# Performance work log

Hardware: AMD Instinct MI355X
Metric: run time of the kernel (lower is better)

## Reference

```python
import jax, jax.numpy as jnp
import numpy as np

H = 16            # num heads
D = 64            # head dim
HID = 1024        # hidden size
ALPHA = 1.0       # < 2 -> power-law kernel
BANDWIDTH = 1.0
A = 0.5           # doubly-stochastic exponent
RADIUS = 1.0      # sphere radius
EPS = 1e-7


def setup_inputs() -> dict:
    key = jax.random.key(0)
    ks = jax.random.split(key, 5)
    x = jax.random.normal(ks[0], (2, 2048, HID), dtype=jnp.float32)
    s = 1.0 / np.sqrt(HID)
    qkv_w = jax.random.normal(ks[1], (3 * HID, HID), dtype=jnp.float32) * s
    qkv_b = jnp.zeros((3 * HID,), dtype=jnp.float32)
    out_w = jax.random.normal(ks[2], (HID, HID), dtype=jnp.float32) * s
    out_b = jnp.zeros((HID,), dtype=jnp.float32)
    return {"x": x, "qkv_w": qkv_w, "qkv_b": qkv_b, "out_w": out_w, "out_b": out_b}


def _l2norm(t):
    # torch F.normalize(p=2, dim=-1): divide by max(||t||, 1e-12)
    n = jnp.sqrt(jnp.sum(t * t, axis=-1, keepdims=True))
    return t / jnp.maximum(n, 1e-12)


def reference(x, qkv_w, qkv_b, out_w, out_b):
    B, S, _ = x.shape
    qkv = x @ qkv_w.T + qkv_b                       # [B,S,3*HID]
    q, k, v = jnp.split(qkv, 3, axis=-1)
    # [B,H,S,D]
    q = _l2norm(q.reshape(B, S, H, D).transpose(0, 2, 1, 3))
    k = _l2norm(k.reshape(B, S, H, D).transpose(0, 2, 1, 3))
    v = v.reshape(B, S, H, D).transpose(0, 2, 1, 3)
    # geodesic distance on the sphere
    cos = jnp.clip(jnp.einsum('bhsd,bhtd->bhst', q, k), -1.0 + EPS, 1.0 - EPS)
    g_dist = jnp.arccos(cos) * RADIUS               # [B,H,S,S]
    # alpha < 2: power-law kernel
    attn_score = (1.0 + g_dist / jnp.sqrt(BANDWIDTH)) ** (-(D + ALPHA))
    # doubly-stochastic-style rescale: diag(row^-a) @ K @ diag(col^-a)
    row = attn_score.sum(-1) ** (-A)                # [B,H,S]
    col = attn_score.sum(-2) ** (-A)                # [B,H,S]
    k_tilde = row[..., :, None] * attn_score * col[..., None, :]
    # F.normalize(p=1, dim=3): divide by max(sum |.|, 1e-12); entries >= 0
    probs = k_tilde / jnp.maximum(k_tilde.sum(-1, keepdims=True), 1e-12)
    out = jnp.einsum('bhst,bhtd->bhsd', probs, v)   # [B,H,S,D]
    out = out.transpose(0, 2, 1, 3).reshape(B, S, HID)
    return out @ out_w.T + out_b
```

## Files before the change

kernel.cpp:

```cpp
#include <hip/hip_runtime.h>
#include <math.h>

#define NH   16
#define HD   64
#define HIDN 1024
#define NB   2
#define SEQ  2048
#define ROWS (NB*SEQ)
#define BH   (NB*NH)

typedef __attribute__((ext_vector_type(8))) short bf16x8;
typedef __attribute__((ext_vector_type(8))) _Float16 f16x8;
typedef __attribute__((ext_vector_type(4))) float f32x4;
typedef _Float16 f16;

typedef const __attribute__((address_space(1))) void GV;
typedef __attribute__((address_space(3))) void LV;
__device__ __forceinline__ void glds16(const void* g, void* l) {
    __builtin_amdgcn_global_load_lds((GV*)g, (LV*)l, 16, 0, 0);
}

__device__ __forceinline__ unsigned short f2bf(float f) {
    unsigned u = __float_as_uint(f);
    u += 0x7FFF + ((u >> 16) & 1);
    return (unsigned short)(u >> 16);
}
__device__ __forceinline__ bf16x8 ldfrag(const unsigned short* p) {
    return *(const bf16x8*)p;
}
__device__ __forceinline__ f16x8 ldfragh(const f16* p) {
    return *(const f16x8*)p;
}
__device__ __forceinline__ f32x4 mfma16(bf16x8 a, bf16x8 b, f32x4 c) {
    return __builtin_amdgcn_mfma_f32_16x16x32_bf16(a, b, c, 0, 0, 0);
}
__device__ __forceinline__ f32x4 mfma16h(f16x8 a, f16x8 b, f32x4 c) {
    return __builtin_amdgcn_mfma_f32_16x16x32_f16(a, b, c, 0, 0, 0);
}

__device__ __forceinline__ float log2_1pacos(float c) {
    float u = fmaxf(1.0f - c, 0.0f);
    float s = __builtin_amdgcn_sqrtf(u);
    float p = fmaf(u, 2.68532e-3f, 7.89259e-3f);
    p = fmaf(u, p, 2.6516504e-2f);
    p = fmaf(u, p, 1.1785113e-1f);
    p = fmaf(u, p, 1.4142136f);
    return __builtin_amdgcn_logf(fmaf(s, p, 1.0f));
}

__global__ __launch_bounds__(256)
void conv_f16(const float* __restrict__ src, f16* __restrict__ dst) {
    int i = (blockIdx.x * 256 + threadIdx.x) * 8;
    float4 a = *(const float4*)(src + i);
    float4 b = *(const float4*)(src + i + 4);
    f16x8 o = { (f16)a.x, (f16)a.y, (f16)a.z, (f16)a.w,
                (f16)b.x, (f16)b.y, (f16)b.z, (f16)b.w };
    *(f16x8*)(dst + i) = o;
}

__global__ __launch_bounds__(256)
void gemm_nt_f16(const f16* __restrict__ A, const f16* __restrict__ B,
                 const float* __restrict__ bias, float* __restrict__ C,
                 int M, int N, int K)
{
    __shared__ f16 As[128 * 32];
    __shared__ f16 Bs[128 * 32];
    const int tid = threadIdx.x;
    const int lane = tid & 63, w = tid >> 6;
    const int ln = lane & 15, lq = lane >> 4;
    const int wm = (w >> 1) * 64, wn = (w & 1) * 64;
    const int m0 = blockIdx.x * 128, n0 = blockIdx.y * 128;

    const int grow = lane >> 2;
    const int gcol = (lane & 3) * 8;
    const f16* Ab = A + (size_t)(m0 + w * 32 + grow) * K + gcol;
    const f16* Bb = B + (size_t)(n0 + w * 32 + grow) * K + gcol;
    f16* Asw = As + (w * 32) * 32;
    f16* Bsw = Bs + (w * 32) * 32;

    f32x4 acc[4][4];
    #pragma unroll
    for (int i = 0; i < 4; ++i)
        #pragma unroll
        for (int j = 0; j < 4; ++j) acc[i][j] = (f32x4){0.f, 0.f, 0.f, 0.f};

    for (int kc = 0; kc < K; kc += 32) {
        __syncthreads();
        #pragma unroll
        for (int i = 0; i < 2; ++i) {
            glds16(Ab + (size_t)(i * 16) * K + kc, Asw + (i * 16) * 32);
            glds16(Bb + (size_t)(i * 16) * K + kc, Bsw + (i * 16) * 32);
        }
        __syncthreads();
        f16x8 af[4], bf[4];
        #pragma unroll
        for (int i = 0; i < 4; ++i)
            af[i] = *(const f16x8*)&As[(wm + i * 16 + ln) * 32 + lq * 8];
        #pragma unroll
        for (int j = 0; j < 4; ++j)
            bf[j] = *(const f16x8*)&Bs[(wn + j * 16 + ln) * 32 + lq * 8];
        #pragma unroll
        for (int i = 0; i < 4; ++i)
            #pragma unroll
            for (int j = 0; j < 4; ++j)
                acc[i][j] = mfma16h(af[i], bf[j], acc[i][j]);
    }

    #pragma unroll
    for (int i = 0; i < 4; ++i) {
        #pragma unroll
        for (int j = 0; j < 4; ++j) {
            int colIdx = n0 + wn + j * 16 + ln;
            float bs = bias[colIdx];
            #pragma unroll
            for (int r = 0; r < 4; ++r) {
                int row = m0 + wm + i * 16 + lq * 4 + r;
                C[(size_t)row * N + colIdx] = acc[i][j][r] + bs;
            }
        }
    }
}

__global__ __launch_bounds__(256)
void normalize_qk_f16(const float* __restrict__ qkv,
                      f16* __restrict__ qf, f16* __restrict__ kf)
{
    int w    = blockIdx.x * 4 + (threadIdx.x >> 6);
    int lane = threadIdx.x & 63;
    int n = w >> 4, h = w & 15;
    int b = n >> 11, s = n & 2047;
    const float* base = qkv + (size_t)n * 3 * HIDN + h * HD;
    float q = base[lane], k = base[HIDN + lane];
    float qs = q * q, ks = k * k;
    #pragma unroll
    for (int o = 32; o; o >>= 1) { qs += __shfl_xor(qs, o); ks += __shfl_xor(ks, o); }
    q *= 1.0f / fmaxf(sqrtf(qs), 1e-12f);
    k *= 1.0f / fmaxf(sqrtf(ks), 1e-12f);
    size_t idx = ((size_t)((b * NH + h) * SEQ + s)) * HD + lane;
    qf[idx] = (f16)q;
    kf[idx] = (f16)k;
}

__global__ __launch_bounds__(256)
void v_transpose(const float* __restrict__ qkv, unsigned short* __restrict__ vth)
{
    __shared__ float Ls[64][65];
    int bh = blockIdx.y, s0 = blockIdx.x * 64;
    int b = bh >> 4, h = bh & 15;
    int tid = threadIdx.x;
    #pragma unroll
    for (int i = 0; i < 4; ++i) {
        int idx = tid + i * 256;
        int row = idx >> 4, c4 = (idx & 15) * 4;
        float4 v = *(const float4*)&qkv[((size_t)(b * SEQ + s0 + row)) * 3 * HIDN
                                        + 2 * HIDN + h * HD + c4];
        Ls[row][c4+0] = v.x; Ls[row][c4+1] = v.y; Ls[row][c4+2] = v.z; Ls[row][c4+3] = v.w;
    }
    __syncthreads();
    int d = tid >> 2, sb = (tid & 3) * 16;
    unsigned short hi[16];
    #pragma unroll
    for (int j = 0; j < 16; ++j) hi[j] = f2bf(Ls[sb + j][d]);
    size_t o = ((size_t)bh * HD + d) * SEQ + s0 + sb;
    *(uint4*)&vth[o]     = *(uint4*)&hi[0];
    *(uint4*)&vth[o + 8] = *(uint4*)&hi[8];
}

#define KSTR 72

__global__ __launch_bounds__(256)
void col_sum_f16(const f16* __restrict__ qf, const f16* __restrict__ kf,
                 float* __restrict__ colp)
{
    __shared__ __align__(16) f16 Qs[64 * KSTR];
    int bh = blockIdx.y;
    int tid = threadIdx.x, w = tid >> 6, lane = tid & 63, ln = lane & 15, lq = lane >> 4;
    int m0 = blockIdx.x * 64 + w * 16;
    const f16* qb = qf + (size_t)bh * SEQ * HD;
    const int sr = tid >> 3;
    const int sc = (tid & 7) * 8;

    size_t rowK = ((size_t)bh * SEQ + m0 + ln) * HD;
    f16x8 kf0 = ldfragh(kf + rowK + lq * 8), kf1 = ldfragh(kf + rowK + 32 + lq * 8);

    uint4 qa = *(const uint4*)(qb + (size_t)sr * HD + sc);
    uint4 qc = *(const uint4*)(qb + (size_t)(sr + 32) * HD + sc);

    float cacc[4] = {0.f, 0.f, 0.f, 0.f};
    #pragma unroll 1
    for (int st = 0; st < SEQ / 64; ++st) {
        __syncthreads();
        *(uint4*)&Qs[sr * KSTR + sc] = qa;
        *(uint4*)&Qs[(sr + 32) * KSTR + sc] = qc;
        int sn = (st + 1 < SEQ / 64) ? (st + 1) * 64 : 0;
        qa = *(const uint4*)(qb + (size_t)(sn + sr) * HD + sc);
        qc = *(const uint4*)(qb + (size_t)(sn + sr + 32) * HD + sc);
        __syncthreads();
        #pragma unroll
        for (int nt = 0; nt < 4; ++nt) {
            const f16* qp = &Qs[(nt * 16 + ln) * KSTR + lq * 8];
            f32x4 sacc = {0.f, 0.f, 0.f, 0.f};
            sacc = mfma16h(kf0, *(const f16x8*)qp, sacc);
            sacc = mfma16h(kf1, *(const f16x8*)(qp + 32), sacc);
            #pragma unroll
            for (int r = 0; r < 4; ++r)
                cacc[r] += __builtin_amdgcn_exp2f(-65.0f * log2_1pacos(sacc[r]));
        }
    }
    #pragma unroll
    for (int r = 0; r < 4; ++r) {
        float v = cacc[r];
        v += __shfl_xor(v, 1); v += __shfl_xor(v, 2);
        v += __shfl_xor(v, 4); v += __shfl_xor(v, 8);
        if (ln == 0)
            colp[(size_t)bh * SEQ + m0 + lq * 4 + r] = v;
    }
}

__global__ __launch_bounds__(256)
void col_finalize(const float* __restrict__ colp, float* __restrict__ col)
{
    int i = (blockIdx.x * 256 + threadIdx.x) * 4;
    float4 a = *(const float4*)&colp[i];
    float4 o;
    o.x = -0.5f * __builtin_amdgcn_logf(a.x);
    o.y = -0.5f * __builtin_amdgcn_logf(a.y);
    o.z = -0.5f * __builtin_amdgcn_logf(a.z);
    o.w = -0.5f * __builtin_amdgcn_logf(a.w);
    *(float4*)&col[i] = o;
}

__global__ __launch_bounds__(256)
void attn_f16(const f16* __restrict__ qf, const f16* __restrict__ kf,
              const unsigned short* __restrict__ vth,
              const float* __restrict__ col, f16* __restrict__ ctx)
{
    __shared__ __align__(16) f16 Ks[64 * KSTR];
    __shared__ __align__(16) unsigned short Vs[64 * KSTR];
    __shared__ __align__(16) unsigned short Ws[4][16 * KSTR];
    __shared__ float lcls[64];
    int bh = blockIdx.y;
    int b = bh >> 4, h = bh & 15;
    int tid = threadIdx.x, w = tid >> 6, lane = tid & 63, ln = lane & 15, lq = lane >> 4;
    int m0 = blockIdx.x * 64 + w * 16;
    unsigned short* ws = Ws[w];

    const f16* kb = kf + (size_t)bh * SEQ * HD;
    const unsigned short* vb = vth + (size_t)bh * HD * SEQ;
    const float* cb = col + (size_t)bh * SEQ;

    const int sr = tid >> 3;
    const int sc = (tid & 7) * 8;

    size_t rowQ = ((size_t)bh * SEQ + m0 + ln) * HD;
    f16x8 qf0 = ldfragh(qf + rowQ + lq * 8), qf1 = ldfragh(qf + rowQ + 32 + lq * 8);

    bf16x8 ones;
    #pragma unroll
    for (int i = 0; i < 8; ++i) ones[i] = (short)0x3F80;

    f32x4 num[4];
    #pragma unroll
    for (int nt = 0; nt < 4; ++nt) num[nt] = (f32x4){0.f, 0.f, 0.f, 0.f};
    f32x4 den = {0.f, 0.f, 0.f, 0.f};

    uint4 ka = *(const uint4*)(kb + (size_t)sr * HD + sc);
    uint4 kc = *(const uint4*)(kb + (size_t)(sr + 32) * HD + sc);
    uint4 va = *(const uint4*)(vb + (size_t)sr * SEQ + sc);
    uint4 vc = *(const uint4*)(vb + (size_t)(sr + 32) * SEQ + sc);
    float clv = (tid < 64) ? cb[tid] : 0.f;

    #pragma unroll 1
    for (int tt = 0; tt < SEQ / 64; ++tt) {
        int t0 = tt * 64;
        __syncthreads();
        *(uint4*)&Ks[sr * KSTR + sc] = ka;
        *(uint4*)&Ks[(sr + 32) * KSTR + sc] = kc;
        *(uint4*)&Vs[sr * KSTR + sc] = va;
        *(uint4*)&Vs[(sr + 32) * KSTR + sc] = vc;
        if (tid < 64) lcls[tid] = clv;
        int tn = (tt + 1 < SEQ / 64) ? (tt + 1) * 64 : 0;
        ka = *(const uint4*)(kb + (size_t)(tn + sr) * HD + sc);
        kc = *(const uint4*)(kb + (size_t)(tn + sr + 32) * HD + sc);
        va = *(const uint4*)(vb + (size_t)sr * SEQ + tn + sc);
        vc = *(const uint4*)(vb + (size_t)(sr + 32) * SEQ + tn + sc);
        clv = (tid < 64) ? cb[tn + tid] : 0.f;
        __syncthreads();

        #pragma unroll
        for (int nt = 0; nt < 4; ++nt) {
            const f16* kp = &Ks[(nt * 16 + ln) * KSTR + lq * 8];
            f32x4 sacc = {0.f, 0.f, 0.f, 0.f};
            sacc = mfma16h(qf0, *(const f16x8*)kp, sacc);
            sacc = mfma16h(qf1, *(const f16x8*)(kp + 32), sacc);
            float lcl = lcls[nt * 16 + ln];
            #pragma unroll
            for (int r = 0; r < 4; ++r) {
                float l = log2_1pacos(sacc[r]);
                float wv = __builtin_amdgcn_exp2f(fmaf(l, -65.0f, lcl));
                ws[(lq * 4 + r) * KSTR + nt * 16 + ln] =
                    (unsigned short)(__float_as_uint(wv) >> 16);
            }
        }
        bf16x8 wa0 = ldfrag(ws + ln * KSTR + lq * 8);
        bf16x8 wa1 = ldfrag(ws + ln * KSTR + 32 + lq * 8);
        den = mfma16(wa0, ones, den);
        den = mfma16(wa1, ones, den);
        #pragma unroll
        for (int nt = 0; nt < 4; ++nt) {
            const unsigned short* vp = &Vs[(nt * 16 + ln) * KSTR + lq * 8];
            num[nt] = mfma16(wa0, *(const bf16x8*)vp, num[nt]);
            num[nt] = mfma16(wa1, *(const bf16x8*)(vp + 32), num[nt]);
        }
    }

    #pragma unroll
    for (int r = 0; r < 4; ++r) {
        float inv = 1.0f / fmaxf(den[r], 1e-12f);
        int s = m0 + lq * 4 + r;
        #pragma unroll
        for (int nt = 0; nt < 4; ++nt)
            ctx[((size_t)(b * SEQ + s)) * HIDN + h * HD + nt * 16 + ln] =
                (f16)(num[nt][r] * inv);
    }
}

extern "C" void kernel_launch(void* const* d_in, const int* in_sizes, int n_in,
                              void* d_out, int out_size, void* d_ws, size_t ws_size,
                              hipStream_t stream) {
    const float* x      = (const float*)d_in[0];
    const float* qkv_w  = (const float*)d_in[1];
    const float* qkv_b  = (const float*)d_in[2];
    const float* out_w  = (const float*)d_in[3];
    const float* out_b  = (const float*)d_in[4];
    float* out = (float*)d_out;

    const size_t NTT = (size_t)BH * SEQ * HD;
    float* qkv = (float*)d_ws;
    float* colp = qkv;
    float* col = qkv + (size_t)ROWS * 3 * HIDN;
    f16* xh    = (f16*)(col + (size_t)BH * SEQ);
    f16* wqh   = xh + (size_t)ROWS * HIDN;
    f16* woh   = wqh + (size_t)3 * HIDN * HIDN;
    f16* ctxh  = woh + (size_t)HIDN * HIDN;
    f16* qfp   = ctxh + (size_t)ROWS * HIDN;
    f16* kfp   = qfp + NTT;
    unsigned short* vth = (unsigned short*)(kfp + NTT);

    conv_f16<<<ROWS*HIDN/2048, 256, 0, stream>>>(x, xh);
    conv_f16<<<3*HIDN*HIDN/2048, 256, 0, stream>>>(qkv_w, wqh);
    conv_f16<<<HIDN*HIDN/2048, 256, 0, stream>>>(out_w, woh);

    gemm_nt_f16<<<dim3(ROWS/128, 3*HIDN/128), 256, 0, stream>>>(
        xh, wqh, qkv_b, qkv, ROWS, 3*HIDN, HIDN);
    normalize_qk_f16<<<ROWS*NH/4, 256, 0, stream>>>(qkv, qfp, kfp);
    v_transpose<<<dim3(SEQ/64, BH), 256, 0, stream>>>(qkv, vth);
    col_sum_f16<<<dim3(SEQ/64, BH), 256, 0, stream>>>(qfp, kfp, colp);
    col_finalize<<<BH*SEQ/1024, 256, 0, stream>>>(colp, col);
    attn_f16<<<dim3(SEQ/64, BH), 256, 0, stream>>>(qfp, kfp, vth, col, ctxh);
    gemm_nt_f16<<<dim3(ROWS/128, HIDN/128), 256, 0, stream>>>(
        ctxh, woh, out_b, out, ROWS, HIDN, HIDN);
}
```

Baseline: 330.4 us.

## Replace log/exp power with rcp and repeated squaring, packed pair math and transposed score tile

```diff
diff --git a/kernel.cpp b/kernel.cpp
--- a/kernel.cpp
+++ b/kernel.cpp
@@ -12,6 +12,7 @@
 typedef __attribute__((ext_vector_type(8))) short bf16x8;
 typedef __attribute__((ext_vector_type(8))) _Float16 f16x8;
 typedef __attribute__((ext_vector_type(4))) float f32x4;
+typedef __attribute__((ext_vector_type(2))) float f32x2;
 typedef _Float16 f16;
 
 typedef const __attribute__((address_space(1))) void GV;
@@ -38,14 +39,25 @@
     return __builtin_amdgcn_mfma_f32_16x16x32_f16(a, b, c, 0, 0, 0);
 }
 
-__device__ __forceinline__ float log2_1pacos(float c) {
-    float u = fmaxf(1.0f - c, 0.0f);
-    float s = __builtin_amdgcn_sqrtf(u);
-    float p = fmaf(u, 2.68532e-3f, 7.89259e-3f);
-    p = fmaf(u, p, 2.6516504e-2f);
-    p = fmaf(u, p, 1.1785113e-1f);
-    p = fmaf(u, p, 1.4142136f);
-    return __builtin_amdgcn_logf(fmaf(s, p, 1.0f));
+__device__ __forceinline__ f32x2 pow65_pair(float c0, float c1) {
+    f32x2 u = { fmaxf(1.0f - c0, 0.0f), fmaxf(1.0f - c1, 0.0f) };
+    f32x2 s = { __builtin_amdgcn_sqrtf(u.x), __builtin_amdgcn_sqrtf(u.y) };
+    f32x2 p = u * 2.68532e-3f + 7.89259e-3f;
+    p = u * p + 2.6516504e-2f;
+    p = u * p + 1.1785113e-1f;
+    p = u * p + 1.4142136f;
+    f32x2 t = s * p + 1.0f;
+    f32x2 y = { __builtin_amdgcn_rcpf(t.x), __builtin_amdgcn_rcpf(t.y) };
+    f32x2 y2  = y  * y;
+    f32x2 y4  = y2 * y2;
+    f32x2 y8  = y4 * y4;
+    f32x2 y16 = y8 * y8;
+    f32x2 y32 = y16 * y16;
+    f32x2 y64 = y32 * y32;
+    return y64 * y;
+}
+__device__ __forceinline__ unsigned packbf(f32x2 w) {
+    return (__float_as_uint(w.x) >> 16) | (__float_as_uint(w.y) & 0xffff0000u);
 }
 
 __global__ __launch_bounds__(256)
@@ -186,7 +198,7 @@
     uint4 qa = *(const uint4*)(qb + (size_t)sr * HD + sc);
     uint4 qc = *(const uint4*)(qb + (size_t)(sr + 32) * HD + sc);
 
-    float cacc[4] = {0.f, 0.f, 0.f, 0.f};
+    f32x2 cacc01 = {0.f, 0.f}, cacc23 = {0.f, 0.f};
     #pragma unroll 1
     for (int st = 0; st < SEQ / 64; ++st) {
         __syncthreads();
@@ -202,11 +214,11 @@
             f32x4 sacc = {0.f, 0.f, 0.f, 0.f};
             sacc = mfma16h(kf0, *(const f16x8*)qp, sacc);
             sacc = mfma16h(kf1, *(const f16x8*)(qp + 32), sacc);
-            #pragma unroll
-            for (int r = 0; r < 4; ++r)
-                cacc[r] += __builtin_amdgcn_exp2f(-65.0f * log2_1pacos(sacc[r]));
-        }
-    }
+            cacc01 += pow65_pair(sacc[0], sacc[1]);
+            cacc23 += pow65_pair(sacc[2], sacc[3]);
+        }
+    }
+    float cacc[4] = {cacc01.x, cacc01.y, cacc23.x, cacc23.y};
     #pragma unroll
     for (int r = 0; r < 4; ++r) {
         float v = cacc[r];
@@ -223,10 +235,10 @@
     int i = (blockIdx.x * 256 + threadIdx.x) * 4;
     float4 a = *(const float4*)&colp[i];
     float4 o;
-    o.x = -0.5f * __builtin_amdgcn_logf(a.x);
-    o.y = -0.5f * __builtin_amdgcn_logf(a.y);
-    o.z = -0.5f * __builtin_amdgcn_logf(a.z);
-    o.w = -0.5f * __builtin_amdgcn_logf(a.w);
+    o.x = __builtin_amdgcn_rsqf(a.x);
+    o.y = __builtin_amdgcn_rsqf(a.y);
+    o.z = __builtin_amdgcn_rsqf(a.z);
+    o.w = __builtin_amdgcn_rsqf(a.w);
     *(float4*)&col[i] = o;
 }
 
@@ -238,7 +250,7 @@
     __shared__ __align__(16) f16 Ks[64 * KSTR];
     __shared__ __align__(16) unsigned short Vs[64 * KSTR];
     __shared__ __align__(16) unsigned short Ws[4][16 * KSTR];
-    __shared__ float lcls[64];
+    __shared__ __align__(16) float lcls[64];
     int bh = blockIdx.y;
     int b = bh >> 4, h = bh & 15;
     int tid = threadIdx.x, w = tid >> 6, lane = tid & 63, ln = lane & 15, lq = lane >> 4;
@@ -272,7 +284,6 @@
 
     #pragma unroll 1
     for (int tt = 0; tt < SEQ / 64; ++tt) {
-        int t0 = tt * 64;
         __syncthreads();
         *(uint4*)&Ks[sr * KSTR + sc] = ka;
         *(uint4*)&Ks[(sr + 32) * KSTR + sc] = kc;
@@ -291,16 +302,15 @@
         for (int nt = 0; nt < 4; ++nt) {
             const f16* kp = &Ks[(nt * 16 + ln) * KSTR + lq * 8];
             f32x4 sacc = {0.f, 0.f, 0.f, 0.f};
-            sacc = mfma16h(qf0, *(const f16x8*)kp, sacc);
-            sacc = mfma16h(qf1, *(const f16x8*)(kp + 32), sacc);
-            float lcl = lcls[nt * 16 + ln];
-            #pragma unroll
-            for (int r = 0; r < 4; ++r) {
-                float l = log2_1pacos(sacc[r]);
-                float wv = __builtin_amdgcn_exp2f(fmaf(l, -65.0f, lcl));
-                ws[(lq * 4 + r) * KSTR + nt * 16 + ln] =
-                    (unsigned short)(__float_as_uint(wv) >> 16);
-            }
+            sacc = mfma16h(*(const f16x8*)kp, qf0, sacc);
+            sacc = mfma16h(*(const f16x8*)(kp + 32), qf1, sacc);
+            float4 cl = *(const float4*)&lcls[nt * 16 + lq * 4];
+            f32x2 w01 = pow65_pair(sacc[0], sacc[1]) * (f32x2){cl.x, cl.y};
+            f32x2 w23 = pow65_pair(sacc[2], sacc[3]) * (f32x2){cl.z, cl.w};
+            uint2 pw;
+            pw.x = packbf(w01);
+            pw.y = packbf(w23);
+            *(uint2*)(ws + ln * KSTR + nt * 16 + lq * 4) = pw;
         }
         bf16x8 wa0 = ldfrag(ws + ln * KSTR + lq * 8);
         bf16x8 wa1 = ldfrag(ws + ln * KSTR + 32 + lq * 8);
```

After: 341.1 us. 1.03x slower.
